# Kernel tuning notes

Hardware: AMD Instinct MI355X
Metric: run time of the kernel (lower is better)

The kernel has to match this reference:

```python
import jax, jax.numpy as jnp
import numpy as np

BN_EPS = 1e-5
NEG_SLOPE = 0.2  # PyG GATConv default negative_slope

N, E, D, H1, H2, OUT = 20000, 320000, 256, 256, 1024, 10


def setup_inputs() -> dict:
    key = jax.random.key(0)
    ks = jax.random.split(key, 16)
    rn = lambda k, s, sc=0.05: jax.random.normal(k, s, jnp.float32) * sc
    return {
        "x": rn(ks[0], (N, D), 1.0),
        "edge_index": jax.random.randint(ks[1], (2, E), 0, N, dtype=jnp.int64),
        "gc1_Ws": rn(ks[2], (D, H1)), "gc1_Wd": rn(ks[3], (D, H1)),
        "gc1_as": rn(ks[4], (H1,)), "gc1_ad": rn(ks[5], (H1,)), "gc1_b": jnp.zeros((H1,)),
        "gc2_Ws": rn(ks[6], (H1, H2)), "gc2_Wd": rn(ks[7], (H1, H2)),
        "gc2_as": rn(ks[8], (H2,)), "gc2_ad": rn(ks[9], (H2,)), "gc2_b": jnp.zeros((H2,)),
        "fc1_W": rn(ks[10], (H2, 4092)), "fc1_b": jnp.zeros((4092,)),
        "bn1_g": jnp.ones((4092,)), "bn1_b": jnp.zeros((4092,)),
        "fc2_W": rn(ks[11], (4092, 1024)), "fc2_b": jnp.zeros((1024,)),
        "bn2_g": jnp.ones((1024,)), "bn2_b": jnp.zeros((1024,)),
        "fc3_W": rn(ks[12], (1024, 256)), "fc3_b": jnp.zeros((256,)),
        "bn3_g": jnp.ones((256,)), "bn3_b": jnp.zeros((256,)),
        "fc4_W": rn(ks[13], (256, OUT)), "fc4_b": jnp.zeros((OUT,)),
    }


def gat_conv(x, src, dst, Ws, Wd, a_s, a_d, b):
    """PyG GATConv, heads=1: lin -> per-node attn logits -> gather ->
    LeakyReLU -> segment softmax over dst -> scatter-add, + bias."""
    n = x.shape[0]
    xs = x @ Ws                     # [N, F] source transform
    xd = x @ Wd                     # [N, F] target transform
    al_s = xs @ a_s                 # [N]
    al_d = xd @ a_d                 # [N]
    e = jax.nn.leaky_relu(al_s[src] + al_d[dst], NEG_SLOPE)   # [E]
    m = jax.ops.segment_max(e, dst, num_segments=n)
    ee = jnp.exp(e - m[dst])
    ssum = jax.ops.segment_sum(ee, dst, num_segments=n)
    alpha = ee / (ssum[dst] + 1e-16)                          # [E]
    out = jax.ops.segment_sum(alpha[:, None] * xs[src], dst, num_segments=n)
    return out + b


def batch_norm(x, g, b):
    mu = x.mean(0)
    var = ((x - mu) ** 2).mean(0)   # biased var, as torch BN training fwd
    return g * (x - mu) * jax.lax.rsqrt(var + BN_EPS) + b


def reference(x, edge_index,
              gc1_Ws, gc1_Wd, gc1_as, gc1_ad, gc1_b,
              gc2_Ws, gc2_Wd, gc2_as, gc2_ad, gc2_b,
              fc1_W, fc1_b, bn1_g, bn1_b,
              fc2_W, fc2_b, bn2_g, bn2_b,
              fc3_W, fc3_b, bn3_g, bn3_b,
              fc4_W, fc4_b):
    n = x.shape[0]
    # GATConv default add_self_loops=True
    loops = jnp.arange(n, dtype=edge_index.dtype)
    src = jnp.concatenate([edge_index[0], loops])
    dst = jnp.concatenate([edge_index[1], loops])

    h = jax.nn.relu(gat_conv(x, src, dst, gc1_Ws, gc1_Wd, gc1_as, gc1_ad, gc1_b))
    h = jax.nn.relu(gat_conv(h, src, dst, gc2_Ws, gc2_Wd, gc2_as, gc2_ad, gc2_b))
    h = jax.nn.relu(batch_norm(h @ fc1_W + fc1_b, bn1_g, bn1_b))
    h = jax.nn.relu(batch_norm(h @ fc2_W + fc2_b, bn2_g, bn2_b))
    h = jax.nn.relu(batch_norm(h @ fc3_W + fc3_b, bn3_g, bn3_b))
    h = h @ fc4_W + fc4_b
    return jax.nn.log_softmax(h, axis=-1)
```

## Files before the change

### kernel.cpp

```cpp
#include <hip/hip_runtime.h>

#define NN 20000
#define EE 320000
#define DD 256
#define HH1 256
#define HH2 1024
#define CC1 4092
#define CC1P 4096
#define OUTC 10
#define EA (EE + NN)

#define CEILDIV(a,b) (((a)+(b)-1)/(b))

typedef unsigned short u16;
typedef __attribute__((ext_vector_type(8))) short bf16x8;
typedef __attribute__((ext_vector_type(4))) float f32x4;

__device__ __forceinline__ float b2f(unsigned short u) {
  union { unsigned int i; float f; } v; v.i = ((unsigned int)u) << 16; return v.f;
}
__device__ __forceinline__ unsigned short f2b(float f) {
  unsigned int x = __float_as_uint(f);
  unsigned int r = (x + 0x7fffu + ((x >> 16) & 1u)) >> 16;
  return (unsigned short)r;
}

__device__ __forceinline__ void gload16(const u16* g, u16* l) {
  __builtin_amdgcn_global_load_lds(
      (const __attribute__((address_space(1))) unsigned int*)(unsigned long long)(const void*)g,
      (__attribute__((address_space(3))) unsigned int*)(unsigned int)(unsigned long long)(void*)l,
      16, 0, 0);
}

__global__ void k_zero32(unsigned int* __restrict__ p, int n) {
  int i = blockIdx.x * 256 + threadIdx.x;
  if (i < n) p[i] = 0u;
}

__global__ void k_f32_to_bf16(const float* __restrict__ in, u16* __restrict__ out, int n) {
  int i = blockIdx.x * 256 + threadIdx.x;
  if (i < n) out[i] = f2b(in[i]);
}

__global__ void k_convT(const float* __restrict__ in, u16* __restrict__ out,
                        int K, int N, int Kp) {
  __shared__ float tile[32][33];
  int kb = blockIdx.y * 32, nb = blockIdx.x * 32;
  int tx = threadIdx.x & 31, ty = threadIdx.x >> 5;
  #pragma unroll
  for (int i = 0; i < 32; i += 8) {
    int k = kb + ty + i, n = nb + tx;
    tile[ty + i][tx] = (k < K && n < N) ? in[(size_t)k * N + n] : 0.f;
  }
  __syncthreads();
  #pragma unroll
  for (int i = 0; i < 32; i += 8) {
    int n = nb + ty + i, k = kb + tx;
    if (n < N && k < Kp) out[(size_t)n * Kp + k] = f2b(tile[tx][ty + i]);
  }
}

__global__ void k_detect_e64(const int* __restrict__ ei, int* __restrict__ flag) {
  __shared__ int nz;
  if (threadIdx.x == 0) nz = 0;
  __syncthreads();
  if (ei[2 * threadIdx.x + 1] != 0) atomicOr(&nz, 1);
  __syncthreads();
  if (threadIdx.x == 0) *flag = (nz == 0) ? 1 : 0;
}

__device__ __forceinline__ int eread(const int* __restrict__ ei, int f64, int idx) {
  return f64 ? ei[(size_t)idx * 2] : ei[idx];
}

__global__ void k_proj_vec(const float* __restrict__ Ws, const float* __restrict__ as_,
                           const float* __restrict__ Wd, const float* __restrict__ ad_,
                           float* __restrict__ ps, float* __restrict__ pd, int K, int F) {
  int k = blockIdx.x;
  if (k >= K) return;
  int lane = threadIdx.x;
  const float* wsr = Ws + (size_t)k * F;
  const float* wdr = Wd + (size_t)k * F;
  float s = 0.f, d = 0.f;
  for (int f = lane * 4; f < F; f += 256) {
    float4 w1 = *(const float4*)(wsr + f);
    float4 a1 = *(const float4*)(as_ + f);
    float4 w2 = *(const float4*)(wdr + f);
    float4 a2 = *(const float4*)(ad_ + f);
    s += w1.x * a1.x + w1.y * a1.y + w1.z * a1.z + w1.w * a1.w;
    d += w2.x * a2.x + w2.y * a2.y + w2.z * a2.z + w2.w * a2.w;
  }
  #pragma unroll
  for (int off = 32; off > 0; off >>= 1) {
    s += __shfl_xor(s, off);
    d += __shfl_xor(d, off);
  }
  if (lane == 0) { ps[k] = s; pd[k] = d; }
}

__global__ void k_attn_logits(const u16* __restrict__ act, const float* __restrict__ ps,
                              const float* __restrict__ pd, float* __restrict__ als,
                              float* __restrict__ ald, int K) {
  int n = blockIdx.x;
  int lane = threadIdx.x;
  const u16* row = act + (size_t)n * K;
  float s = 0.f, d = 0.f;
  for (int k = lane; k < K; k += 64) {
    float v = b2f(row[k]);
    s += v * ps[k]; d += v * pd[k];
  }
  #pragma unroll
  for (int off = 32; off > 0; off >>= 1) { s += __shfl_down(s, off); d += __shfl_down(d, off); }
  if (lane == 0) { als[n] = s; ald[n] = d; }
}

__global__ void k_edge_count(const int* __restrict__ ei, const int* __restrict__ eflag,
                             int* __restrict__ counts) {
  int k = blockIdx.x * 256 + threadIdx.x;
  if (k >= EA) return;
  int f64 = *eflag;
  int dst = (k < EE) ? eread(ei, f64, EE + k) : (k - EE);
  if ((unsigned)dst < (unsigned)NN) atomicAdd(&counts[dst], 1);
}

__global__ void k_scan(const int* __restrict__ counts, int* __restrict__ rowptr,
                       int* __restrict__ cursor, int n) {
  __shared__ int sdata[1024];
  __shared__ int s_carry;
  if (threadIdx.x == 0) s_carry = 0;
  __syncthreads();
  for (int base = 0; base < n; base += 1024) {
    int idx = base + threadIdx.x;
    int v = (idx < n) ? counts[idx] : 0;
    sdata[threadIdx.x] = v;
    __syncthreads();
    for (int off = 1; off < 1024; off <<= 1) {
      int t = (threadIdx.x >= off) ? sdata[threadIdx.x - off] : 0;
      __syncthreads();
      sdata[threadIdx.x] += t;
      __syncthreads();
    }
    int incl = sdata[threadIdx.x];
    int carry = s_carry;
    if (idx < n) { int e = carry + incl - v; rowptr[idx] = e; cursor[idx] = e; }
    __syncthreads();
    if (threadIdx.x == 1023) s_carry = carry + sdata[1023];
    __syncthreads();
  }
  if (threadIdx.x == 0) rowptr[n] = s_carry;
}

__global__ void k_edge_fill(const int* __restrict__ ei, const int* __restrict__ eflag,
                            int* __restrict__ cursor, int* __restrict__ esrc) {
  int k = blockIdx.x * 256 + threadIdx.x;
  if (k >= EA) return;
  int f64 = *eflag;
  int src, dst;
  if (k < EE) { src = eread(ei, f64, k); dst = eread(ei, f64, EE + k); }
  else { src = dst = k - EE; }
  if ((unsigned)dst >= (unsigned)NN) return;
  if ((unsigned)src >= (unsigned)NN) src = 0;
  int pos = atomicAdd(&cursor[dst], 1);
  esrc[pos] = src;
}

template<int FPT>
__global__ __launch_bounds__(256) void k_gat_aggregate(
    const int* __restrict__ rowptr, const int* __restrict__ esrc,
    const float* __restrict__ als, const float* __restrict__ ald,
    const u16* __restrict__ xs, const float* __restrict__ bias,
    u16* __restrict__ h, int F) {
  int n = blockIdx.x;
  int beg = rowptr[n], end = rowptr[n + 1];
  float ad = ald[n];
  float m = -1e30f;
  for (int j = beg; j < end; ++j) {
    float e = als[esrc[j]] + ad; e = (e < 0.f) ? 0.2f * e : e;
    m = fmaxf(m, e);
  }
  float ssum = 0.f;
  for (int j = beg; j < end; ++j) {
    float e = als[esrc[j]] + ad; e = (e < 0.f) ? 0.2f * e : e;
    ssum += expf(e - m);
  }
  float inv = 1.f / (ssum + 1e-16f);
  float acc[FPT];
  #pragma unroll
  for (int i = 0; i < FPT; ++i) acc[i] = 0.f;
  int fbase = threadIdx.x * FPT;
  for (int j = beg; j < end; ++j) {
    int s = esrc[j];
    float e = als[s] + ad; e = (e < 0.f) ? 0.2f * e : e;
    float alpha = expf(e - m) * inv;
    const u16* rowp = xs + (size_t)s * F + fbase;
    if (FPT == 4) {
      ushort4 v4 = *(const ushort4*)rowp;
      acc[0] += alpha * b2f(v4.x);
      acc[1] += alpha * b2f(v4.y);
      acc[2] += alpha * b2f(v4.z);
      acc[3] += alpha * b2f(v4.w);
    } else {
      acc[0] += alpha * b2f(rowp[0]);
    }
  }
  #pragma unroll
  for (int i = 0; i < FPT; ++i) {
    int f = fbase + i;
    float v = acc[i] + bias[f];
    h[(size_t)n * F + f] = f2b(v > 0.f ? v : 0.f);
  }
}

template<bool BIAS, bool STATS>
__global__ __launch_bounds__(256, 2) void k_mfma_gemm(
    const u16* __restrict__ A, const u16* __restrict__ Bt,
    const float* __restrict__ bias, u16* __restrict__ C,
    int M, int N, int K, int ldc, int nbx,
    float* __restrict__ bsum, float* __restrict__ bsumsq) {
  __shared__ u16 lds[16384];
  int tid = threadIdx.x;
  int lane = tid & 63;
  int w = tid >> 6;

  int nwg = gridDim.x;
  int id = blockIdx.x;
  int q = nwg >> 3, r = nwg & 7;
  int xcd = id & 7, pos = id >> 3;
  int swz = (xcd < r ? xcd * (q + 1) : r * (q + 1) + (xcd - r) * q) + pos;
  int m0 = (swz / nbx) * 128, n0 = (swz % nbx) * 128;

  int dr = lane >> 2;
  int ss = (lane & 3) ^ ((lane >> 3) & 3);
  int lrow = lane & 15;
  int lk = lane >> 4;

  f32x4 acc[4][4] = {};
  int c0 = w * 4;

  auto STAGE = [&](int k0, int bufb) {
    #pragma unroll
    for (int j = 0; j < 4; ++j) {
      int c = c0 + j;
      int tr = ((c & 7) << 4) + dr;
      const u16* src;
      if (c < 8) {
        int rr = m0 + tr; rr = (rr < M) ? rr : (M - 1);
        src = A + (size_t)rr * K + k0 + ss * 8;
      } else {
        int rr = n0 + tr; rr = (rr < N) ? rr : (N - 1);
        src = Bt + (size_t)rr * K + k0 + ss * 8;
      }
      gload16(src, (u16*)((char*)lds + bufb + c * 1024));
    }
  };
  auto COMPUTE = [&](int bufb) {
    bf16x8 af[4], bfr[4];
    #pragma unroll
    for (int m = 0; m < 4; ++m) {
      int row = ((w >> 1) << 6) + m * 16 + lrow;
      af[m] = *(const bf16x8*)((const char*)lds + bufb + row * 64 +
                               ((lk ^ ((row >> 1) & 3)) << 4));
    }
    #pragma unroll
    for (int n = 0; n < 4; ++n) {
      int row = ((w & 1) << 6) + n * 16 + lrow;
      bfr[n] = *(const bf16x8*)((const char*)lds + bufb + 8192 + row * 64 +
                                ((lk ^ ((row >> 1) & 3)) << 4));
    }
    #pragma unroll
    for (int m = 0; m < 4; ++m)
      #pragma unroll
      for (int n = 0; n < 4; ++n)
        acc[m][n] = __builtin_amdgcn_mfma_f32_16x16x32_bf16(af[m], bfr[n], acc[m][n], 0, 0, 0);
  };

  int cur = 0;
  STAGE(0, 0);
  asm volatile("s_waitcnt vmcnt(0)" ::: "memory");
  __syncthreads();
  for (int k0 = 32; k0 < K; k0 += 32) {
    STAGE(k0, (cur ^ 1) * 16384);
    COMPUTE(cur * 16384);
    asm volatile("s_waitcnt vmcnt(0)" ::: "memory");
    __syncthreads();
    cur ^= 1;
  }
  COMPUTE(cur * 16384);

  int wrb = (w >> 1) * 64, wcb = (w & 1) * 64;
  float colS[4] = {0.f, 0.f, 0.f, 0.f}, colS2[4] = {0.f, 0.f, 0.f, 0.f};
  #pragma unroll
  for (int m = 0; m < 4; ++m) {
    #pragma unroll
    for (int qq = 0; qq < 4; ++qq) {
      int gm = m0 + wrb + m * 16 + lk * 4 + qq;
      bool okm = gm < M;
      #pragma unroll
      for (int n = 0; n < 4; ++n) {
        int gn = n0 + wcb + n * 16 + lrow;
        if (gn >= N) continue;
        float v = acc[m][n][qq];
        if (BIAS) v += bias[gn];
        if (okm) {
          C[(size_t)gm * ldc + gn] = f2b(v);
          if (STATS) { colS[n] += v; colS2[n] += v * v; }
        }
      }
    }
  }
  if (STATS) {
    __syncthreads();
    float* ls = (float*)lds;
    ls[tid] = 0.f;
    __syncthreads();
    #pragma unroll
    for (int n = 0; n < 4; ++n) {
      int col = wcb + n * 16 + lrow;
      atomicAdd(&ls[col], colS[n]);
      atomicAdd(&ls[128 + col], colS2[n]);
    }
    __syncthreads();
    if (tid < 128) {
      int gn = n0 + tid;
      if (gn < N) {
        atomicAdd(&bsum[gn], ls[tid]);
        atomicAdd(&bsumsq[gn], ls[128 + tid]);
      }
    }
  }
}

__global__ void k_bn_finalize(const float* __restrict__ sum, const float* __restrict__ sumsq,
                              float* __restrict__ mu, float* __restrict__ rs, int C, float invN) {
  int c = blockIdx.x * 256 + threadIdx.x;
  if (c >= C) return;
  float m = sum[c] * invN;
  float var = fmaxf(sumsq[c] * invN - m * m, 0.f);
  mu[c] = m; rs[c] = rsqrtf(var + 1e-5f);
}

__global__ void k_bn_apply_relu(u16* __restrict__ h, const float* __restrict__ mu,
                                const float* __restrict__ rs, const float* __restrict__ g,
                                const float* __restrict__ b, long total4, int Ccols, int ld) {
  long i = (long)blockIdx.x * 256 + threadIdx.x;
  if (i >= total4) return;
  long e = i * 4;
  int c = (int)(e % Ccols);
  long r = e / Ccols;
  u16* p = h + (size_t)r * ld + c;
  ushort4 v = *(ushort4*)p;
  float f0 = b2f(v.x), f1 = b2f(v.y), f2 = b2f(v.z), f3 = b2f(v.w);
  f0 = g[c + 0] * (f0 - mu[c + 0]) * rs[c + 0] + b[c + 0];
  f1 = g[c + 1] * (f1 - mu[c + 1]) * rs[c + 1] + b[c + 1];
  f2 = g[c + 2] * (f2 - mu[c + 2]) * rs[c + 2] + b[c + 2];
  f3 = g[c + 3] * (f3 - mu[c + 3]) * rs[c + 3] + b[c + 3];
  v.x = f2b(f0 > 0.f ? f0 : 0.f);
  v.y = f2b(f1 > 0.f ? f1 : 0.f);
  v.z = f2b(f2 > 0.f ? f2 : 0.f);
  v.w = f2b(f3 > 0.f ? f3 : 0.f);
  *(ushort4*)p = v;
}

__global__ void k_fc4_logsoftmax(const u16* __restrict__ h, const float* __restrict__ W,
                                 const float* __restrict__ b, float* __restrict__ out) {
  int n = blockIdx.x;
  int lane = threadIdx.x;
  const u16* row = h + (size_t)n * HH1;
  float hv[4];
  #pragma unroll
  for (int j = 0; j < 4; ++j) hv[j] = b2f(row[lane + j * 64]);
  float logits[OUTC];
  #pragma unroll
  for (int o = 0; o < OUTC; ++o) {
    float p = 0.f;
    #pragma unroll
    for (int j = 0; j < 4; ++j) p += hv[j] * W[(size_t)(lane + j * 64) * OUTC + o];
    #pragma unroll
    for (int off = 32; off > 0; off >>= 1) p += __shfl_down(p, off);
    logits[o] = p;
  }
  if (lane == 0) {
    float mx = -1e30f;
    #pragma unroll
    for (int o = 0; o < OUTC; ++o) { logits[o] += b[o]; mx = fmaxf(mx, logits[o]); }
    float se = 0.f;
    #pragma unroll
    for (int o = 0; o < OUTC; ++o) se += expf(logits[o] - mx);
    float ls = mx + logf(se);
    #pragma unroll
    for (int o = 0; o < OUTC; ++o) out[(size_t)n * OUTC + o] = logits[o] - ls;
  }
}

extern "C" void kernel_launch(void* const* d_in, const int* in_sizes, int n_in,
                              void* d_out, int out_size, void* d_ws, size_t ws_size,
                              hipStream_t stream) {
  const float* x    = (const float*)d_in[0];
  const int*   ei   = (const int*)d_in[1];
  const float* g1Ws = (const float*)d_in[2];
  const float* g1Wd = (const float*)d_in[3];
  const float* g1as = (const float*)d_in[4];
  const float* g1ad = (const float*)d_in[5];
  const float* g1b  = (const float*)d_in[6];
  const float* g2Ws = (const float*)d_in[7];
  const float* g2Wd = (const float*)d_in[8];
  const float* g2as = (const float*)d_in[9];
  const float* g2ad = (const float*)d_in[10];
  const float* g2b  = (const float*)d_in[11];
  const float* f1W  = (const float*)d_in[12];
  const float* f1b  = (const float*)d_in[13];
  const float* bn1g = (const float*)d_in[14];
  const float* bn1b = (const float*)d_in[15];
  const float* f2W  = (const float*)d_in[16];
  const float* f2b_ = (const float*)d_in[17];
  const float* bn2g = (const float*)d_in[18];
  const float* bn2b = (const float*)d_in[19];
  const float* f3W  = (const float*)d_in[20];
  const float* f3b  = (const float*)d_in[21];
  const float* bn3g = (const float*)d_in[22];
  const float* bn3b = (const float*)d_in[23];
  const float* f4W  = (const float*)d_in[24];
  const float* f4b  = (const float*)d_in[25];
  float* out = (float*)d_out;
  (void)in_sizes; (void)n_in; (void)out_size; (void)ws_size;

  char* Wb = (char*)d_ws;
  size_t off = 0;
  auto alloc = [&](size_t bytes) -> char* {
    char* p = Wb + off;
    off = (off + bytes + 255) & ~(size_t)255;
    return p;
  };
  u16* h3   = (u16*)Wb;
  u16* xs2  = (u16*)alloc((size_t)NN * HH2 * 2);
  u16* xs1  = (u16*)alloc((size_t)NN * HH1 * 2);
  u16* xb   = (u16*)alloc((size_t)NN * DD * 2);
  u16* h1   = (u16*)alloc((size_t)NN * HH1 * 2);
  u16* h5   = (u16*)alloc((size_t)NN * HH1 * 2);
  u16* Bt1  = (u16*)alloc((size_t)HH1 * DD * 2);
  u16* Bt2  = (u16*)alloc((size_t)HH2 * HH1 * 2);
  int* esrc   = (int*)alloc((size_t)EA * 4);
  int* rowptr = (int*)alloc((NN + 1) * 4);
  int* cursor = (int*)alloc(NN * 4);
  int* counts = (int*)alloc(NN * 4);
  float* als1 = (float*)alloc(NN * 4);
  float* ald1 = (float*)alloc(NN * 4);
  float* als2 = (float*)alloc(NN * 4);
  float* ald2 = (float*)alloc(NN * 4);
  float* ps1  = (float*)alloc(1024 * 4);
  float* pd1  = (float*)alloc(1024 * 4);
  float* ps2  = (float*)alloc(1024 * 4);
  float* pd2  = (float*)alloc(1024 * 4);
  int* eflag  = (int*)alloc(256);

  off = ((size_t)NN * CC1P * 2 + 255) & ~(size_t)255;
  u16* h2 = (u16*)alloc((size_t)NN * HH2 * 2);
  u16* h4 = h2;
  u16* Bf = (u16*)alloc((size_t)HH2 * CC1P * 2);
  float* bsum   = (float*)alloc((size_t)CC1 * 2 * 4);
  float* bsumsq = bsum + CC1;
  float* bmu    = (float*)alloc((size_t)CC1 * 4);
  float* brs    = (float*)alloc((size_t)CC1 * 4);

  k_f32_to_bf16<<<CEILDIV(NN * DD, 256), 256, 0, stream>>>(x, xb, NN * DD);

  k_detect_e64<<<1, 256, 0, stream>>>(ei, eflag);
  k_zero32<<<CEILDIV(NN, 256), 256, 0, stream>>>((unsigned int*)counts, NN);
  k_edge_count<<<CEILDIV(EA, 256), 256, 0, stream>>>(ei, eflag, counts);
  k_scan<<<1, 1024, 0, stream>>>(counts, rowptr, cursor, NN);
  k_edge_fill<<<CEILDIV(EA, 256), 256, 0, stream>>>(ei, eflag, cursor, esrc);

  k_convT<<<dim3(CEILDIV(HH1, 32), CEILDIV(DD, 32)), 256, 0, stream>>>(g1Ws, Bt1, DD, HH1, DD);
  k_proj_vec<<<DD, 64, 0, stream>>>(g1Ws, g1as, g1Wd, g1ad, ps1, pd1, DD, HH1);
  k_attn_logits<<<NN, 64, 0, stream>>>(xb, ps1, pd1, als1, ald1, DD);
  k_mfma_gemm<false, false><<<CEILDIV(HH1, 128) * CEILDIV(NN, 128), 256, 0, stream>>>(
      xb, Bt1, nullptr, xs1, NN, HH1, DD, HH1, CEILDIV(HH1, 128), nullptr, nullptr);
  k_gat_aggregate<1><<<NN, 256, 0, stream>>>(rowptr, esrc, als1, ald1, xs1, g1b, h1, HH1);

  k_convT<<<dim3(CEILDIV(HH2, 32), CEILDIV(HH1, 32)), 256, 0, stream>>>(g2Ws, Bt2, HH1, HH2, HH1);
  k_proj_vec<<<HH1, 64, 0, stream>>>(g2Ws, g2as, g2Wd, g2ad, ps2, pd2, HH1, HH2);
  k_attn_logits<<<NN, 64, 0, stream>>>(h1, ps2, pd2, als2, ald2, HH1);
  k_mfma_gemm<false, false><<<CEILDIV(HH2, 128) * CEILDIV(NN, 128), 256, 0, stream>>>(
      h1, Bt2, nullptr, xs2, NN, HH2, HH1, HH2, CEILDIV(HH2, 128), nullptr, nullptr);
  k_gat_aggregate<4><<<NN, 256, 0, stream>>>(rowptr, esrc, als2, ald2, xs2, g2b, h2, HH2);

  k_convT<<<dim3(CEILDIV(CC1, 32), CEILDIV(HH2, 32)), 256, 0, stream>>>(f1W, Bf, HH2, CC1, HH2);
  k_zero32<<<CEILDIV(2 * CC1, 256), 256, 0, stream>>>((unsigned int*)bsum, 2 * CC1);
  k_mfma_gemm<true, true><<<CEILDIV(CC1, 128) * CEILDIV(NN, 128), 256, 0, stream>>>(
      h2, Bf, f1b, h3, NN, CC1, HH2, CC1P, CEILDIV(CC1, 128), bsum, bsumsq);
  k_bn_finalize<<<CEILDIV(CC1, 256), 256, 0, stream>>>(bsum, bsumsq, bmu, brs, CC1, 1.f / NN);
  k_bn_apply_relu<<<CEILDIV((long)NN * CC1 / 4, 256), 256, 0, stream>>>(
      h3, bmu, brs, bn1g, bn1b, (long)NN * CC1 / 4, CC1, CC1P);

  k_convT<<<dim3(CEILDIV(HH2, 32), CEILDIV(CC1P, 32)), 256, 0, stream>>>(f2W, Bf, CC1, HH2, CC1P);
  k_zero32<<<CEILDIV(2 * CC1, 256), 256, 0, stream>>>((unsigned int*)bsum, 2 * CC1);
  k_mfma_gemm<true, true><<<CEILDIV(HH2, 128) * CEILDIV(NN, 128), 256, 0, stream>>>(
      h3, Bf, f2b_, h4, NN, HH2, CC1P, HH2, CEILDIV(HH2, 128), bsum, bsumsq);
  k_bn_finalize<<<CEILDIV(HH2, 256), 256, 0, stream>>>(bsum, bsumsq, bmu, brs, HH2, 1.f / NN);
  k_bn_apply_relu<<<CEILDIV((long)NN * HH2 / 4, 256), 256, 0, stream>>>(
      h4, bmu, brs, bn2g, bn2b, (long)NN * HH2 / 4, HH2, HH2);

  k_convT<<<dim3(CEILDIV(HH1, 32), CEILDIV(HH2, 32)), 256, 0, stream>>>(f3W, Bf, HH2, HH1, HH2);
  k_zero32<<<CEILDIV(2 * CC1, 256), 256, 0, stream>>>((unsigned int*)bsum, 2 * CC1);
  k_mfma_gemm<true, true><<<CEILDIV(HH1, 128) * CEILDIV(NN, 128), 256, 0, stream>>>(
      h4, Bf, f3b, h5, NN, HH1, HH2, HH1, CEILDIV(HH1, 128), bsum, bsumsq);
  k_bn_finalize<<<CEILDIV(HH1, 256), 256, 0, stream>>>(bsum, bsumsq, bmu, brs, HH1, 1.f / NN);
  k_bn_apply_relu<<<CEILDIV((long)NN * HH1 / 4, 256), 256, 0, stream>>>(
      h5, bmu, brs, bn3g, bn3b, (long)NN * HH1 / 4, HH1, HH1);

  k_fc4_logsoftmax<<<NN, 64, 0, stream>>>(h5, f4W, f4b, out);
}
```

Before: 1.080 ms.

## Parallelize GAT softmax over edges with block reductions and LDS-staged alphas

Each GAT aggregation block previously had all 256 threads redundantly walk every incoming edge three times to compute the segment max, the sum and the per-edge alpha serially. The max and sum are now computed with edges strided across threads followed by shared-memory tree reductions. Alphas and source indices are precomputed in chunks into LDS so the feature accumulation loop only reads them. This removes redundant gathers and expf work but adds several __syncthreads per node, and average degree is only about 17.

```diff
diff --git a/kernel.cpp b/kernel.cpp
--- a/kernel.cpp
+++ b/kernel.cpp
@@ -164,44 +164,75 @@
   esrc[pos] = src;
 }
 
+#define ACHUNK 512
 template<int FPT>
 __global__ __launch_bounds__(256) void k_gat_aggregate(
     const int* __restrict__ rowptr, const int* __restrict__ esrc,
     const float* __restrict__ als, const float* __restrict__ ald,
     const u16* __restrict__ xs, const float* __restrict__ bias,
     u16* __restrict__ h, int F) {
+  __shared__ float red[256];
+  __shared__ float salpha[ACHUNK];
+  __shared__ int   ssrc[ACHUNK];
   int n = blockIdx.x;
+  int tid = threadIdx.x;
   int beg = rowptr[n], end = rowptr[n + 1];
   float ad = ald[n];
+
   float m = -1e30f;
-  for (int j = beg; j < end; ++j) {
+  for (int j = beg + tid; j < end; j += 256) {
     float e = als[esrc[j]] + ad; e = (e < 0.f) ? 0.2f * e : e;
     m = fmaxf(m, e);
   }
-  float ssum = 0.f;
-  for (int j = beg; j < end; ++j) {
+  red[tid] = m; __syncthreads();
+  #pragma unroll
+  for (int s = 128; s > 0; s >>= 1) {
+    if (tid < s) red[tid] = fmaxf(red[tid], red[tid + s]);
+    __syncthreads();
+  }
+  m = red[0]; __syncthreads();
+
+  float ss = 0.f;
+  for (int j = beg + tid; j < end; j += 256) {
     float e = als[esrc[j]] + ad; e = (e < 0.f) ? 0.2f * e : e;
-    ssum += expf(e - m);
-  }
-  float inv = 1.f / (ssum + 1e-16f);
+    ss += expf(e - m);
+  }
+  red[tid] = ss; __syncthreads();
+  #pragma unroll
+  for (int s = 128; s > 0; s >>= 1) {
+    if (tid < s) red[tid] += red[tid + s];
+    __syncthreads();
+  }
+  float inv = 1.f / (red[0] + 1e-16f); __syncthreads();
+
   float acc[FPT];
   #pragma unroll
   for (int i = 0; i < FPT; ++i) acc[i] = 0.f;
-  int fbase = threadIdx.x * FPT;
-  for (int j = beg; j < end; ++j) {
-    int s = esrc[j];
-    float e = als[s] + ad; e = (e < 0.f) ? 0.2f * e : e;
-    float alpha = expf(e - m) * inv;
-    const u16* rowp = xs + (size_t)s * F + fbase;
-    if (FPT == 4) {
-      ushort4 v4 = *(const ushort4*)rowp;
-      acc[0] += alpha * b2f(v4.x);
-      acc[1] += alpha * b2f(v4.y);
-      acc[2] += alpha * b2f(v4.z);
-      acc[3] += alpha * b2f(v4.w);
-    } else {
-      acc[0] += alpha * b2f(rowp[0]);
-    }
+  int fbase = tid * FPT;
+  for (int cbeg = beg; cbeg < end; cbeg += ACHUNK) {
+    int cend = min(cbeg + ACHUNK, end);
+    for (int j = cbeg + tid; j < cend; j += 256) {
+      int s = esrc[j];
+      float e = als[s] + ad; e = (e < 0.f) ? 0.2f * e : e;
+      salpha[j - cbeg] = expf(e - m) * inv;
+      ssrc[j - cbeg] = s;
+    }
+    __syncthreads();
+    int cn = cend - cbeg;
+    for (int j = 0; j < cn; ++j) {
+      float a = salpha[j];
+      const u16* rowp = xs + (size_t)ssrc[j] * F + fbase;
+      if (FPT == 4) {
+        ushort4 v4 = *(const ushort4*)rowp;
+        acc[0] += a * b2f(v4.x);
+        acc[1] += a * b2f(v4.y);
+        acc[2] += a * b2f(v4.z);
+        acc[3] += a * b2f(v4.w);
+      } else {
+        acc[0] += a * b2f(rowp[0]);
+      }
+    }
+    __syncthreads();
   }
   #pragma unroll
   for (int i = 0; i < FPT; ++i) {
```

Result: faster. 954.0 us (-11.7%).
